# Performance work log

Measured on AMD Instinct MI355X. Metric: run time of the kernel, lower is better.

Reference implementation:

```python
import jax, jax.numpy as jnp
import numpy as np

N_NODES = 50000
N_EDGES = 800000
IN_F, HID, OUT, FC_OUT = 192, 128, 64, 192


def setup_inputs() -> dict:
    key = jax.random.key(0)
    ks = jax.random.split(key, 12)
    s = 0.05
    return {
        "x": jax.random.normal(ks[0], (N_NODES, IN_F), dtype=jnp.float32),
        "edge_index": jax.random.randint(ks[1], (2, N_EDGES), 0, N_NODES, dtype=jnp.int64),
        "W1": jax.random.normal(ks[2], (IN_F, HID), dtype=jnp.float32) * s,
        "b1": jnp.zeros((HID,), jnp.float32),
        "Wg": jax.random.normal(ks[3], (HID, HID), dtype=jnp.float32) * s,
        "a_src": jax.random.normal(ks[4], (HID,), dtype=jnp.float32) * s,
        "a_dst": jax.random.normal(ks[5], (HID,), dtype=jnp.float32) * s,
        "bg": jnp.zeros((HID,), jnp.float32),
        "W2": jax.random.normal(ks[6], (HID, OUT), dtype=jnp.float32) * s,
        "b2": jnp.zeros((OUT,), jnp.float32),
        "Wf": jax.random.normal(ks[7], (OUT, FC_OUT), dtype=jnp.float32) * s,
        "bf": jnp.zeros((FC_OUT,), jnp.float32),
    }


def reference(x, edge_index, W1, b1, Wg, a_src, a_dst, bg, W2, b2, Wf, bf):
    N = x.shape[0]
    loops = jnp.arange(N, dtype=edge_index.dtype)
    src = jnp.concatenate([edge_index[0], loops])  # [E+N]
    dst = jnp.concatenate([edge_index[1], loops])

    # GCN symmetric normalization with self-loops (PyG gcn_norm)
    deg = jax.ops.segment_sum(jnp.ones_like(dst, dtype=x.dtype), dst, num_segments=N)
    dinv = jax.lax.rsqrt(jnp.maximum(deg, 1.0))  # deg >= 1 due to self-loops
    norm = dinv[src] * dinv[dst]  # [E+N]

    def gcn(h, W, b):
        h = h @ W
        out = jax.ops.segment_sum(h[src] * norm[:, None], dst, num_segments=N)
        return out + b

    h = gcn(x, W1, b1)  # [N, HID]

    # GAT layer (1 head, PyG defaults: self-loops, LeakyReLU(0.2), softmax over dst)
    hg = h @ Wg
    al = hg @ a_src  # [N]
    ar = hg @ a_dst  # [N]
    e = jax.nn.leaky_relu(al[src] + ar[dst], 0.2)  # [E+N]
    emax = jax.ops.segment_max(e, dst, num_segments=N)
    ex = jnp.exp(e - emax[dst])
    denom = jax.ops.segment_sum(ex, dst, num_segments=N)
    alpha = ex / denom[dst]
    h = jax.ops.segment_sum(hg[src] * alpha[:, None], dst, num_segments=N) + bg

    h = jax.nn.relu(h)
    h = gcn(h, W2, b2)  # [N, OUT]
    return h @ Wf + bf  # [N, 192]
```

## Files before the change

### kernel.cpp

```cpp
#include <hip/hip_runtime.h>
#include <hip/hip_fp16.h>
#include <cstdint>
#include <cstddef>

#define NN 50000
#define NE 800000
#define RNG 8
#define RSZ ((NN + RNG - 1) / RNG)
#define FIL_CPR 256
#define FILB (RNG*FIL_CPR)
#define CAP 64

typedef _Float16 half8 __attribute__((ext_vector_type(8)));
typedef float    f32x4 __attribute__((ext_vector_type(4)));

static __device__ __forceinline__ float lrelu02(float x){ return x > 0.f ? x : 0.2f*x; }

static __device__ __forceinline__ float2 h2f(uint32_t u){
  __half2 h = *reinterpret_cast<__half2*>(&u);
  return __half22float2(h);
}
static __device__ __forceinline__ uint32_t f2h(float a, float b){
  __half2 h = __floats2half2_rn(a, b);
  return *reinterpret_cast<uint32_t*>(&h);
}
static __device__ __forceinline__ void acc8p(float* acc, uint4 raw, float p){
  float2 f0=h2f(raw.x), f1=h2f(raw.y), f2=h2f(raw.z), f3=h2f(raw.w);
  acc[0]+=p*f0.x; acc[1]+=p*f0.y; acc[2]+=p*f1.x; acc[3]+=p*f1.y;
  acc[4]+=p*f2.x; acc[5]+=p*f2.y; acc[6]+=p*f3.x; acc[7]+=p*f3.y;
}
static __device__ __forceinline__ void acc8s(float* acc, uint4 raw){
  float2 f0=h2f(raw.x), f1=h2f(raw.y), f2=h2f(raw.z), f3=h2f(raw.w);
  acc[0]+=f0.x; acc[1]+=f0.y; acc[2]+=f1.x; acc[3]+=f1.y;
  acc[4]+=f2.x; acc[5]+=f2.y; acc[6]+=f3.x; acc[7]+=f3.y;
}

__global__ __launch_bounds__(256) void pack_all_kernel(
    const float* __restrict__ W1, const float* __restrict__ Wg,
    const float* __restrict__ W2, const float* __restrict__ Wf,
    const float* __restrict__ b1,
    _Float16* __restrict__ B1, _Float16* __restrict__ B3, _Float16* __restrict__ B4,
    float* __restrict__ bg1, int* __restrict__ fillp)
{
  const int b = blockIdx.x;
  if (b >= 176){
    if (b < 372){
      const int i = (b - 176)*256 + threadIdx.x;
      if (i < NN) fillp[i] = 0;
    } else {
      const int n = threadIdx.x;
      if (n < 128){
        float s = 0.f;
        #pragma unroll 4
        for (int c = 0; c < 128; ++c) s += b1[c]*Wg[c*128 + n];
        bg1[n] = s;
      }
    }
    return;
  }
  const float* B; _Float16* O; int K, N, base; bool fused = false;
  if      (b < 96)  { B = W1; O = B1; K = 192; N = 128; base = 0;  fused = true; }
  else if (b < 128) { B = W2; O = B3; K = 128; N = 64;  base = 96;  }
  else              { B = Wf; O = B4; K = 64;  N = 192; base = 128; }
  const int i = (b - base)*256 + threadIdx.x;
  if (i >= K*N) return;
  const int j    = i & 7;
  const int lane = (i >> 3) & 63;
  const int tile = i >> 9;
  const int ntl  = N >> 4;
  const int ct   = tile % ntl;
  const int k0   = (tile / ntl) << 5;
  const int k = k0 + ((lane >> 4) << 3) + j;
  const int n = (ct << 4) + (lane & 15);
  if (fused){
    float s = 0.f;
    #pragma unroll 4
    for (int c = 0; c < 128; ++c) s += W1[k*128 + c]*Wg[c*128 + n];
    O[i] = (_Float16)s;
  } else {
    O[i] = (_Float16)B[(size_t)k*N + n];
  }
}

template<int K, int NT, bool AHALF, bool HALF_OUT, bool RSLEN>
static __device__ __forceinline__ void gemm_block(
    const void* __restrict__ Av, const _Float16* __restrict__ Bsw,
    const float* __restrict__ bias, const int* __restrict__ rslen,
    void* __restrict__ Cv, int M, int N, int bm, int t)
{
  constexpr int NTL = NT*4;
  const int w    = t >> 6;
  const int lane = t & 63;
  const int m    = lane & 15;
  const int quad = lane >> 4;

  f32x4 acc[NTL];
  #pragma unroll
  for (int ct = 0; ct < NTL; ++ct) acc[ct] = (f32x4){0.f,0.f,0.f,0.f};

  const int row = bm + w*16 + m;
  const _Float16* bp = Bsw + lane*8;

  #pragma unroll
  for (int k0 = 0; k0 < K; k0 += 32){
    union { half8 h; uint4 u; uint32_t w[4]; } ua;
    if constexpr (AHALF){
      if (row < M){
        ua.u = *(const uint4*)((const _Float16*)Av + (size_t)row*K + k0 + quad*8);
      } else {
        ua.u = make_uint4(0u,0u,0u,0u);
      }
    } else {
      if (row < M){
        const float* Arow = (const float*)Av + (size_t)row*K;
        const float4 va = *(const float4*)(Arow + k0 + quad*8);
        const float4 vb = *(const float4*)(Arow + k0 + quad*8 + 4);
        ua.w[0] = f2h(va.x, va.y);
        ua.w[1] = f2h(va.z, va.w);
        ua.w[2] = f2h(vb.x, vb.y);
        ua.w[3] = f2h(vb.z, vb.w);
      } else {
        ua.u = make_uint4(0u,0u,0u,0u);
      }
    }
    const half8 af = ua.h;
    #pragma unroll
    for (int ct = 0; ct < NTL; ++ct){
      const half8 bf = *(const half8*)(bp + ((size_t)((k0>>5)*NTL + ct))*512);
      acc[ct] = __builtin_amdgcn_mfma_f32_16x16x32_f16(af, bf, acc[ct], 0, 0, 0);
    }
  }

  float rs[4];
  #pragma unroll
  for (int reg = 0; reg < 4; ++reg){
    const int r = bm + w*16 + quad*4 + reg;
    rs[reg] = 1.f;
    if constexpr (RSLEN){ if (r < M) rs[reg] = rsqrtf((float)(rslen[r] + 1)); }
  }
  #pragma unroll
  for (int ct = 0; ct < NTL; ++ct){
    const int colg = ct*16 + m;
    const float bv = bias ? bias[colg] : 0.f;
    #pragma unroll
    for (int reg = 0; reg < 4; ++reg){
      const int r = bm + w*16 + quad*4 + reg;
      if (r < M){
        const float v = rs[reg]*acc[ct][reg] + bv;
        if constexpr (HALF_OUT){
          ((__half*)Cv)[(size_t)r*N + colg] = __float2half(v);
        } else {
          ((float*)Cv)[(size_t)r*N + colg] = v;
        }
      }
    }
  }
}

template<int K, int NT, bool AHALF, bool HALF_OUT, bool RSLEN>
__global__ __launch_bounds__(256) void gemm_mfma_kernel(
    const void* __restrict__ Av, const _Float16* __restrict__ Bsw,
    const float* __restrict__ bias, const int* __restrict__ rslen,
    void* __restrict__ Cv, int M, int N)
{
  gemm_block<K,NT,AHALF,HALF_OUT,RSLEN>(Av, Bsw, bias, rslen, Cv, M, N,
                                        blockIdx.x*64, threadIdx.x);
}

__global__ __launch_bounds__(256) void gemm1_fill_kernel(
    const float* __restrict__ A, const _Float16* __restrict__ B1,
    __half* __restrict__ C, int M, int gm,
    const int* __restrict__ src, const int* __restrict__ dst,
    int* __restrict__ fillp, int* __restrict__ col, int E)
{
  if (blockIdx.x < (unsigned)gm){
    gemm_block<192,2,false,true,false>(A, B1, nullptr, nullptr, C, M, 128,
                                       blockIdx.x*64, threadIdx.x);
    return;
  }
  const int fb = blockIdx.x - gm;
  const int r  = fb % RNG;
  const int i  = fb / RNG;
  const int lo = r * RSZ;
  const int hi = min(lo + RSZ, NN);
  const int cs = (E + FIL_CPR - 1) / FIL_CPR;
  const int e1 = min((i+1)*cs, E);
  int e = i*cs + threadIdx.x;
  for (; e + 768 < e1; e += 1024){
    const int d0 = dst[e];       const int d1 = dst[e+256];
    const int d2 = dst[e+512];   const int d3 = dst[e+768];
    const int s0 = src[e];       const int s1 = src[e+256];
    const int s2 = src[e+512];   const int s3 = src[e+768];
    if (d0 >= lo && d0 < hi){ col[(d0<<6) + atomicAdd(&fillp[d0],1)] = s0; }
    if (d1 >= lo && d1 < hi){ col[(d1<<6) + atomicAdd(&fillp[d1],1)] = s1; }
    if (d2 >= lo && d2 < hi){ col[(d2<<6) + atomicAdd(&fillp[d2],1)] = s2; }
    if (d3 >= lo && d3 < hi){ col[(d3<<6) + atomicAdd(&fillp[d3],1)] = s3; }
  }
  for (; e < e1; e += 256){
    const int d = dst[e];
    if (d >= lo && d < hi){ col[(d<<6) + atomicAdd(&fillp[d],1)] = src[e]; }
  }
}

__global__ __launch_bounds__(256) void agg1_kernel(
    const __half* __restrict__ T, const int* __restrict__ len, const int* __restrict__ col,
    const float* __restrict__ bg1, const float* __restrict__ avs,
    const float* __restrict__ avd,
    __half* __restrict__ hg, float* __restrict__ al, float* __restrict__ ar, int N)
{
  const int t  = threadIdx.x;
  const int n  = blockIdx.x * 16 + (t >> 4);
  const int gl = t & 15;
  if (n >= N) return;
  const int ln = len[n];
  const float dn = rsqrtf((float)(ln + 1));
  float acc[8];
  {
    uint4 raw = *(const uint4*)(T + (size_t)n*128 + gl*8);
    float2 f0=h2f(raw.x), f1=h2f(raw.y), f2=h2f(raw.z), f3=h2f(raw.w);
    acc[0]=dn*f0.x; acc[1]=dn*f0.y; acc[2]=dn*f1.x; acc[3]=dn*f1.y;
    acc[4]=dn*f2.x; acc[5]=dn*f2.y; acc[6]=dn*f3.x; acc[7]=dn*f3.y;
  }
  const int s0 = n << 6;
  const int s1 = s0 + ln;
  for (int c0 = s0; c0 < s1; c0 += 16){
    const int nc = min(16, s1 - c0);
    int   sl = (gl < nc) ? col[c0 + gl] : 0;
    float dl = (gl < nc) ? rsqrtf((float)(len[sl] + 1)) : 0.f;
    #pragma unroll 4
    for (int j = 0; j < nc; ++j){
      const int   s = __shfl(sl, j, 16);
      const float p = __shfl(dl, j, 16);
      acc8p(acc, *(const uint4*)(T + (size_t)s*128 + gl*8), p);
    }
  }
  const float* bp = bg1 + gl*8;
  float v[8];
  #pragma unroll
  for (int i = 0; i < 8; ++i) v[i] = dn*acc[i] + bp[i];
  uint4 o;
  o.x = f2h(v[0], v[1]); o.y = f2h(v[2], v[3]);
  o.z = f2h(v[4], v[5]); o.w = f2h(v[6], v[7]);
  *(uint4*)(hg + (size_t)n*128 + gl*8) = o;
  const float* asp = avs + gl*8;
  const float* adp = avd + gl*8;
  float sal = 0.f, sar = 0.f;
  #pragma unroll
  for (int i = 0; i < 8; ++i){ sal += v[i]*asp[i]; sar += v[i]*adp[i]; }
  #pragma unroll
  for (int off = 8; off > 0; off >>= 1){
    sal += __shfl_xor(sal, off, 16);
    sar += __shfl_xor(sar, off, 16);
  }
  if (gl == 0){ al[n] = sal; ar[n] = sar; }
}

__global__ __launch_bounds__(256) void gat_agg_kernel(
    const __half* __restrict__ HG, const int* __restrict__ len, const int* __restrict__ col,
    const float* __restrict__ al, const float* __restrict__ ar,
    const float* __restrict__ bias, __half* __restrict__ out, int N)
{
  const int t  = threadIdx.x;
  const int n  = blockIdx.x * 16 + (t >> 4);
  const int gl = t & 15;
  if (n >= N) return;
  const float arn = ar[n];
  const float pself = __expf(lrelu02(al[n] + arn));
  float lpart = 0.f;
  float acc[8];
  {
    uint4 raw = *(const uint4*)(HG + (size_t)n*128 + gl*8);
    float2 f0=h2f(raw.x), f1=h2f(raw.y), f2=h2f(raw.z), f3=h2f(raw.w);
    acc[0]=pself*f0.x; acc[1]=pself*f0.y; acc[2]=pself*f1.x; acc[3]=pself*f1.y;
    acc[4]=pself*f2.x; acc[5]=pself*f2.y; acc[6]=pself*f3.x; acc[7]=pself*f3.y;
  }
  const int s0 = n << 6;
  const int s1 = s0 + len[n];
  for (int c0 = s0; c0 < s1; c0 += 16){
    const int nc = min(16, s1 - c0);
    int   sl = (gl < nc) ? col[c0 + gl] : 0;
    float pl = (gl < nc) ? __expf(lrelu02(al[sl] + arn)) : 0.f;
    lpart += pl;
    #pragma unroll 4
    for (int j = 0; j < nc; ++j){
      const int   s = __shfl(sl, j, 16);
      const float p = __shfl(pl, j, 16);
      acc8p(acc, *(const uint4*)(HG + (size_t)s*128 + gl*8), p);
    }
  }
  #pragma unroll
  for (int off = 8; off > 0; off >>= 1) lpart += __shfl_xor(lpart, off, 16);
  const float inv = 1.f / (pself + lpart);
  const float* bp = bias + gl*8;
  float4 b0 = *(const float4*)(bp);
  float4 b1 = *(const float4*)(bp + 4);
  uint4 o;
  o.x = f2h(fmaxf(acc[0]*inv + b0.x, 0.f), fmaxf(acc[1]*inv + b0.y, 0.f));
  o.y = f2h(fmaxf(acc[2]*inv + b0.z, 0.f), fmaxf(acc[3]*inv + b0.w, 0.f));
  o.z = f2h(fmaxf(acc[4]*inv + b1.x, 0.f), fmaxf(acc[5]*inv + b1.y, 0.f));
  o.w = f2h(fmaxf(acc[6]*inv + b1.z, 0.f), fmaxf(acc[7]*inv + b1.w, 0.f));
  *(uint4*)(out + (size_t)n*128 + gl*8) = o;
}

__global__ __launch_bounds__(256) void gcn_agg64_kernel(
    const __half* __restrict__ H, const int* __restrict__ len, const int* __restrict__ col,
    const float* __restrict__ bias, __half* __restrict__ out, int N)
{
  const int t  = threadIdx.x;
  const int n  = blockIdx.x * 32 + (t >> 3);
  const int gl = t & 7;
  if (n >= N) return;
  const int ln = len[n];
  const float dn = rsqrtf((float)(ln + 1));
  float acc[8];
  {
    uint4 raw = *(const uint4*)(H + (size_t)n*64 + gl*8);
    float2 f0=h2f(raw.x), f1=h2f(raw.y), f2=h2f(raw.z), f3=h2f(raw.w);
    acc[0]=f0.x; acc[1]=f0.y; acc[2]=f1.x; acc[3]=f1.y;
    acc[4]=f2.x; acc[5]=f2.y; acc[6]=f3.x; acc[7]=f3.y;
  }
  const int s0 = n << 6;
  const int s1 = s0 + ln;
  for (int c0 = s0; c0 < s1; c0 += 8){
    const int nc = min(8, s1 - c0);
    int sl = (gl < nc) ? col[c0 + gl] : 0;
    #pragma unroll 4
    for (int j = 0; j < nc; ++j){
      const int s = __shfl(sl, j, 8);
      acc8s(acc, *(const uint4*)(H + (size_t)s*64 + gl*8));
    }
  }
  const float* bp = bias + gl*8;
  float4 b0 = *(const float4*)(bp);
  float4 b1 = *(const float4*)(bp + 4);
  uint4 o;
  o.x = f2h(dn*acc[0] + b0.x, dn*acc[1] + b0.y);
  o.y = f2h(dn*acc[2] + b0.z, dn*acc[3] + b0.w);
  o.z = f2h(dn*acc[4] + b1.x, dn*acc[5] + b1.y);
  o.w = f2h(dn*acc[6] + b1.z, dn*acc[7] + b1.w);
  *(uint4*)(out + (size_t)n*64 + gl*8) = o;
}

extern "C" void kernel_launch(void* const* d_in, const int* in_sizes, int n_in,
                              void* d_out, int out_size, void* d_ws, size_t ws_size,
                              hipStream_t stream)
{
  const float* x     = (const float*)d_in[0];
  const int*   ei    = (const int*)d_in[1];
  const float* W1    = (const float*)d_in[2];
  const float* b1    = (const float*)d_in[3];
  const float* Wg    = (const float*)d_in[4];
  const float* a_src = (const float*)d_in[5];
  const float* a_dst = (const float*)d_in[6];
  const float* bg    = (const float*)d_in[7];
  const float* W2    = (const float*)d_in[8];
  const float* b2    = (const float*)d_in[9];
  const float* Wf    = (const float*)d_in[10];
  const float* bf    = (const float*)d_in[11];
  const int N = NN, E = NE;
  const int* src = ei;
  const int* dst = ei + E;

  char* p = (char*)d_ws;
  auto alloc = [&](size_t bytes)->char*{
    char* r = p; p += (bytes + 511) & ~size_t(511); return r;
  };
  int*      fillp = (int*)     alloc((size_t)N*4);
  int*      col   = (int*)     alloc((size_t)N*CAP*4);
  float*    alar_ = (float*)   alloc((size_t)N*8);
  __half*   HA    = (__half*)  alloc((size_t)N*128*2);
  __half*   HB    = (__half*)  alloc((size_t)N*128*2);
  _Float16* B1    = (_Float16*)alloc(24576*2);
  _Float16* B3    = (_Float16*)alloc(8192*2);
  _Float16* B4    = (_Float16*)alloc(12288*2);
  float*    bg1   = (float*)   alloc(128*4);
  float*    al    = alar_;
  float*    ar    = alar_ + N;

  const int gm  = (N + 63) / 64;
  const int g16 = (N + 15) / 16;
  const int g32 = (N + 31) / 32;

  pack_all_kernel<<<373, 256, 0, stream>>>(
      W1, Wg, W2, Wf, b1, B1, B3, B4, bg1, fillp);

  gemm1_fill_kernel<<<gm + FILB, 256, 0, stream>>>(
      x, B1, HA, N, gm, src, dst, fillp, col, E);

  agg1_kernel<<<g16, 256, 0, stream>>>(HA, fillp, col, bg1, a_src, a_dst,
                                       HB, al, ar, N);
  gat_agg_kernel<<<g16, 256, 0, stream>>>(HB, fillp, col, al, ar, bg, HA, N);
  gemm_mfma_kernel<128,1,true,true,true><<<gm, 256, 0, stream>>>(
      HA, B3, nullptr, fillp, HB, N, 64);
  gcn_agg64_kernel<<<g32, 256, 0, stream>>>(HB, fillp, col, b2, HA, N);
  gemm_mfma_kernel<64,3,true,false,false><<<gm, 256, 0, stream>>>(
      HA, B4, bf, nullptr, d_out, N, 192);
}
```

Measured before the change: 264.0 us.

## Fuse second GCN aggregation with final FC GEMM via shared-memory tile

Merges the 64-wide GCN aggregation kernel and the final 64x192 MFMA GEMM into one kernel. Each block aggregates 64 nodes into an fp16 tile in LDS, then runs the GEMM from LDS and writes fp32 output with bias. This removes one launch and the global write and re-read of the intermediate N x 64 half buffer. The cost is fewer blocks in the gather phase (64 nodes per block instead of 32) and a serial dependency inside each block between the gather and the MFMA phase.

```diff
diff --git a/kernel.cpp b/kernel.cpp
--- a/kernel.cpp
+++ b/kernel.cpp
@@ -302,43 +302,82 @@
   *(uint4*)(out + (size_t)n*128 + gl*8) = o;
 }
 
-__global__ __launch_bounds__(256) void gcn_agg64_kernel(
+__global__ __launch_bounds__(256) void agg2_gemm4_kernel(
     const __half* __restrict__ H, const int* __restrict__ len, const int* __restrict__ col,
-    const float* __restrict__ bias, __half* __restrict__ out, int N)
-{
+    const float* __restrict__ b2, const _Float16* __restrict__ B4,
+    const float* __restrict__ bf, float* __restrict__ out, int M)
+{
+  __shared__ __align__(16) _Float16 Ah[64][72];
+  const int bm = blockIdx.x * 64;
   const int t  = threadIdx.x;
-  const int n  = blockIdx.x * 32 + (t >> 3);
+
+  const int g  = t >> 3;
   const int gl = t & 7;
-  if (n >= N) return;
-  const int ln = len[n];
-  const float dn = rsqrtf((float)(ln + 1));
-  float acc[8];
-  {
-    uint4 raw = *(const uint4*)(H + (size_t)n*64 + gl*8);
-    float2 f0=h2f(raw.x), f1=h2f(raw.y), f2=h2f(raw.z), f3=h2f(raw.w);
-    acc[0]=f0.x; acc[1]=f0.y; acc[2]=f1.x; acc[3]=f1.y;
-    acc[4]=f2.x; acc[5]=f2.y; acc[6]=f3.x; acc[7]=f3.y;
-  }
-  const int s0 = n << 6;
-  const int s1 = s0 + ln;
-  for (int c0 = s0; c0 < s1; c0 += 8){
-    const int nc = min(8, s1 - c0);
-    int sl = (gl < nc) ? col[c0 + gl] : 0;
-    #pragma unroll 4
-    for (int j = 0; j < nc; ++j){
-      const int s = __shfl(sl, j, 8);
-      acc8s(acc, *(const uint4*)(H + (size_t)s*64 + gl*8));
-    }
-  }
-  const float* bp = bias + gl*8;
-  float4 b0 = *(const float4*)(bp);
-  float4 b1 = *(const float4*)(bp + 4);
-  uint4 o;
-  o.x = f2h(dn*acc[0] + b0.x, dn*acc[1] + b0.y);
-  o.y = f2h(dn*acc[2] + b0.z, dn*acc[3] + b0.w);
-  o.z = f2h(dn*acc[4] + b1.x, dn*acc[5] + b1.y);
-  o.w = f2h(dn*acc[6] + b1.z, dn*acc[7] + b1.w);
-  *(uint4*)(out + (size_t)n*64 + gl*8) = o;
+  #pragma unroll
+  for (int half = 0; half < 2; ++half){
+    const int lr = g + half*32;
+    const int n  = bm + lr;
+    uint4 o = make_uint4(0u,0u,0u,0u);
+    if (n < M){
+      const int ln = len[n];
+      const float dn = rsqrtf((float)(ln + 1));
+      float acc[8];
+      {
+        uint4 raw = *(const uint4*)(H + (size_t)n*64 + gl*8);
+        float2 f0=h2f(raw.x), f1=h2f(raw.y), f2=h2f(raw.z), f3=h2f(raw.w);
+        acc[0]=f0.x; acc[1]=f0.y; acc[2]=f1.x; acc[3]=f1.y;
+        acc[4]=f2.x; acc[5]=f2.y; acc[6]=f3.x; acc[7]=f3.y;
+      }
+      const int s0 = n << 6;
+      const int s1 = s0 + ln;
+      for (int c0 = s0; c0 < s1; c0 += 8){
+        const int nc = min(8, s1 - c0);
+        int sl = (gl < nc) ? col[c0 + gl] : 0;
+        #pragma unroll 4
+        for (int j = 0; j < nc; ++j){
+          const int s = __shfl(sl, j, 8);
+          acc8s(acc, *(const uint4*)(H + (size_t)s*64 + gl*8));
+        }
+      }
+      const float* bp = b2 + gl*8;
+      o.x = f2h(dn*acc[0] + bp[0], dn*acc[1] + bp[1]);
+      o.y = f2h(dn*acc[2] + bp[2], dn*acc[3] + bp[3]);
+      o.z = f2h(dn*acc[4] + bp[4], dn*acc[5] + bp[5]);
+      o.w = f2h(dn*acc[6] + bp[6], dn*acc[7] + bp[7]);
+    }
+    *(uint4*)&Ah[lr][gl*8] = o;
+  }
+  __syncthreads();
+
+  const int w    = t >> 6;
+  const int lane = t & 63;
+  const int m    = lane & 15;
+  const int quad = lane >> 4;
+  f32x4 acc[12];
+  #pragma unroll
+  for (int ct = 0; ct < 12; ++ct) acc[ct] = (f32x4){0.f,0.f,0.f,0.f};
+  const _Float16* bpB = B4 + lane*8;
+  #pragma unroll
+  for (int k0 = 0; k0 < 64; k0 += 32){
+    const half8 af = *(const half8*)&Ah[w*16 + m][k0 + quad*8];
+    #pragma unroll
+    for (int ct = 0; ct < 12; ++ct){
+      const half8 bfr = *(const half8*)(bpB + ((size_t)((k0>>5)*12 + ct))*512);
+      acc[ct] = __builtin_amdgcn_mfma_f32_16x16x32_f16(af, bfr, acc[ct], 0, 0, 0);
+    }
+  }
+  #pragma unroll
+  for (int ct = 0; ct < 12; ++ct){
+    const int colg = ct*16 + m;
+    const float bv = bf[colg];
+    #pragma unroll
+    for (int reg = 0; reg < 4; ++reg){
+      const int r = bm + w*16 + quad*4 + reg;
+      if (r < M){
+        out[(size_t)r*192 + colg] = acc[ct][reg] + bv;
+      }
+    }
+  }
 }
 
 extern "C" void kernel_launch(void* const* d_in, const int* in_sizes, int n_in,
@@ -379,7 +418,6 @@
 
   const int gm  = (N + 63) / 64;
   const int g16 = (N + 15) / 16;
-  const int g32 = (N + 31) / 32;
 
   pack_all_kernel<<<373, 256, 0, stream>>>(
       W1, Wg, W2, Wf, b1, B1, B3, B4, bg1, fillp);
@@ -392,7 +430,6 @@
   gat_agg_kernel<<<g16, 256, 0, stream>>>(HB, fillp, col, al, ar, bg, HA, N);
   gemm_mfma_kernel<128,1,true,true,true><<<gm, 256, 0, stream>>>(
       HA, B3, nullptr, fillp, HB, N, 64);
-  gcn_agg64_kernel<<<g32, 256, 0, stream>>>(HB, fillp, col, b2, HA, N);
-  gemm_mfma_kernel<64,3,true,false,false><<<gm, 256, 0, stream>>>(
-      HA, B4, bf, nullptr, d_out, N, 192);
-}
+  agg2_gemm4_kernel<<<gm, 256, 0, stream>>>(HB, fillp, col, b2, B4, bf,
+                                            (float*)d_out, N);
+}
```

Result: no change. 267.6 us (+1.4%).
